# Optimization experiments

Hardware: AMD Instinct MI355X
Metric: run time of the kernel (lower is better)

The kernel has to match this reference:

```python
import jax, jax.numpy as jnp
import numpy as np

B, N, M, D_IN, D_OUT, H = 4, 2048, 2048, 512, 512, 8
HD = D_OUT // H
LN_EPS = 1e-5


def setup_inputs() -> dict:
    key = jax.random.key(0)
    ks = jax.random.split(key, 10)
    query = jax.random.normal(ks[0], (B, N, D_IN), dtype=jnp.float32)
    kee = jax.random.normal(ks[1], (B, M, D_IN), dtype=jnp.float32)
    val = jax.random.normal(ks[2], (B, M, D_IN), dtype=jnp.float32)
    mask = jax.random.randint(ks[3], (B, N, M), 0, 2, dtype=jnp.int32)
    # xavier_uniform with gain 1/sqrt(2): limit = gain * sqrt(6/(fan_in+fan_out))
    lim = (1.0 / np.sqrt(2.0)) * np.sqrt(6.0 / (D_IN + D_OUT))
    WQ = jax.random.uniform(ks[4], (D_OUT, D_IN), jnp.float32, -lim, lim)
    WK = jax.random.uniform(ks[5], (D_OUT, D_IN), jnp.float32, -lim, lim)
    WV = jax.random.uniform(ks[6], (D_OUT, D_IN), jnp.float32, -lim, lim)
    limO = (1.0 / np.sqrt(2.0)) * np.sqrt(6.0 / (D_OUT + D_OUT))
    WO = jax.random.uniform(ks[7], (D_OUT, D_OUT), jnp.float32, -limO, limO)
    bO = jnp.zeros((D_OUT,), jnp.float32)
    gamma = jnp.ones((D_OUT,), jnp.float32)
    beta = jnp.zeros((D_OUT,), jnp.float32)
    return {"query": query, "key": kee, "value": val, "mask": mask,
            "WQ": WQ, "WK": WK, "WV": WV, "WO": WO, "bO": bO,
            "gamma": gamma, "beta": beta}


def reference(query, key, value, mask, WQ, WK, WV, WO, bO, gamma, beta):
    scale = jnp.float32(1.0 / np.sqrt(HD))
    # project and split heads: [B, H, S, HD]
    Q = (query @ WQ.T).reshape(B, N, H, HD).transpose(0, 2, 1, 3)
    K = (key @ WK.T).reshape(B, M, H, HD).transpose(0, 2, 1, 3)
    V = (value @ WV.T).reshape(B, M, H, HD).transpose(0, 2, 1, 3)
    attn = jnp.einsum('bhnd,bhmd->bhnm', Q, K) * scale
    attn = jnp.where(mask[:, None, :, :] == 0, -jnp.inf, attn)
    attn = jax.nn.softmax(attn, axis=-1)  # dropout is identity in eval
    out = jnp.einsum('bhnm,bhmd->bhnd', attn, V)
    out = out.transpose(0, 2, 1, 3).reshape(B, N, D_OUT)
    out = out @ WO.T + bO
    x = out + query  # residual_proj is Identity (input_dim == output_dim)
    mu = jnp.mean(x, axis=-1, keepdims=True)
    var = jnp.var(x, axis=-1, keepdims=True)
    return (x - mu) * jax.lax.rsqrt(var + LN_EPS) * gamma + beta
```

## Files before the change

### kernel.cpp

```cpp
#include <hip/hip_runtime.h>
#include <stdint.h>

#define B_   4
#define N_   2048
#define M_   2048
#define DIN  512
#define DOUT 512
#define H_   8
#define HD_  64
#define ROWS (B_ * N_)

typedef __attribute__((ext_vector_type(8))) short bf16x8;
typedef __attribute__((ext_vector_type(4))) float f32x4;
typedef __attribute__((ext_vector_type(2))) unsigned int u32x2;
typedef __attribute__((ext_vector_type(4))) unsigned short u16x4;
typedef unsigned short u16;
typedef unsigned int   u32;

#if __has_builtin(__builtin_amdgcn_exp2f)
#define EXP2(x) __builtin_amdgcn_exp2f(x)
#else
#define EXP2(x) exp2f(x)
#endif

__device__ __forceinline__ u16 f2bf(float x) {
  union { float f; u32 u; } v; v.f = x;
  u32 r = (v.u + 0x7FFFu + ((v.u >> 16) & 1u)) >> 16;
  return (u16)r;
}

__device__ __forceinline__ float bf2f(u16 x) {
  union { u32 u; float f; } v; v.u = ((u32)x) << 16;
  return v.f;
}

__device__ __forceinline__ u32 pkbf(float a, float b) {
  u32 r;
  asm("v_cvt_pk_bf16_f32 %0, %1, %2" : "=v"(r) : "v"(a), "v"(b));
  return r;
}

__device__ __forceinline__ void gld16(u16* lds, const u16* g) {
  __builtin_amdgcn_global_load_lds((const __attribute__((address_space(1))) u32*)g,
                                   (__attribute__((address_space(3))) u32*)lds, 16, 0, 0);
}

__global__ __launch_bounds__(256) void k_prep(
    const float* __restrict__ q, const float* __restrict__ k, const float* __restrict__ v,
    const float* __restrict__ wq_, const float* __restrict__ wk_,
    const float* __restrict__ wv_, const float* __restrict__ wo_,
    const int* __restrict__ mask,
    u16* __restrict__ qb, u16* __restrict__ kb, u16* __restrict__ vb,
    u16* __restrict__ wqb, u16* __restrict__ wkb, u16* __restrict__ wvb, u16* __restrict__ wob,
    u32* __restrict__ mbits)
{
  const int id = blockIdx.x;
  if (id >= 6656) {
    const int id2 = id - 6656;
    const int lane = threadIdx.x & 63;
    const int gw = id2 * 4 + (threadIdx.x >> 6);
    #pragma unroll
    for (int it2 = 0; it2 < 4; ++it2) {
      long pos = ((long)gw * 4 + it2) * 64 + lane;
      int mv = mask[pos];
      unsigned long long bal = __ballot(mv != 0);
      if ((lane & 31) == 0) mbits[pos >> 5] = (u32)(bal >> lane);
    }
    return;
  }
  const float* s; u16* d; size_t i;
  if (id < 6144) {
    const int seg = id >> 11;
    s = seg == 0 ? q : seg == 1 ? k : v;
    d = seg == 0 ? qb : seg == 1 ? kb : vb;
    i = (size_t)(id & 2047) * 2048 + threadIdx.x * 8;
  } else {
    const int wid = id - 6144;
    const int seg = wid >> 7;
    s = seg == 0 ? wq_ : seg == 1 ? wk_ : seg == 2 ? wv_ : wo_;
    d = seg == 0 ? wqb : seg == 1 ? wkb : seg == 2 ? wvb : wob;
    i = (size_t)(wid & 127) * 2048 + threadIdx.x * 8;
  }
  f32x4 x = *(const f32x4*)(s + i);
  f32x4 y = *(const f32x4*)(s + i + 4);
  bf16x8 r;
  r[0] = (short)f2bf(x[0]); r[1] = (short)f2bf(x[1]);
  r[2] = (short)f2bf(x[2]); r[3] = (short)f2bf(x[3]);
  r[4] = (short)f2bf(y[0]); r[5] = (short)f2bf(y[1]);
  r[6] = (short)f2bf(y[2]); r[7] = (short)f2bf(y[3]);
  *(bf16x8*)(d + i) = r;
}

__global__ __launch_bounds__(256) void k_gemm_qkv(
    const u16* __restrict__ Aq, const u16* __restrict__ Ak, const u16* __restrict__ Av,
    const u16* __restrict__ Wq, const u16* __restrict__ Wk, const u16* __restrict__ Wv,
    u16* __restrict__ Qo, u16* __restrict__ Ko, u16* __restrict__ Vt)
{
  __shared__ __align__(16) u16 At[2][128 * 64];
  __shared__ __align__(16) u16 Bt[2][128 * 64];
  const int z = blockIdx.z;
  const u16* A = z == 0 ? Aq : z == 1 ? Ak : Av;
  const u16* W = z == 0 ? Wq : z == 1 ? Wk : Wv;
  const int bm = blockIdx.y, bn = blockIdx.x;
  const int t = threadIdx.x, l = t & 63;
  const int w = t >> 6, wr = w >> 1, wc = w & 1;
  const int l15 = l & 15, lg = l >> 4;
  f32x4 acc[4][4] = {};
  const u16* ga = A + (size_t)(bm * 128 + (t >> 3)) * DIN + (t & 7) * 8;
  const u16* gb = W + (size_t)(bn * 128 + (t >> 3)) * DIN + (t & 7) * 8;

  #define STG(buf_, k0_) do {                                           \
    u16* la_ = &At[buf_][t * 8];                                        \
    u16* lb_ = &Bt[buf_][t * 8];                                        \
    _Pragma("unroll")                                                   \
    for (int s2 = 0; s2 < 4; ++s2) {                                    \
      gld16(la_ + s2 * 2048, ga + (size_t)s2 * 32 * DIN + (k0_));       \
      gld16(lb_ + s2 * 2048, gb + (size_t)s2 * 32 * DIN + (k0_));       \
    }                                                                   \
  } while (0)

  STG(0, 0);
  __syncthreads();
  for (int kt = 0; kt < 8; ++kt) {
    const int buf = kt & 1;
    if (kt + 1 < 8) STG(buf ^ 1, (kt + 1) * 64);
    const u16* rowT = (z < 2) ? &Bt[buf][wc * 64 * 64] : &At[buf][wr * 64 * 64];
    const u16* colT = (z < 2) ? &At[buf][wr * 64 * 64] : &Bt[buf][wc * 64 * 64];
    bf16x8 rf[4][2], cf[4][2];
    #pragma unroll
    for (int i = 0; i < 4; ++i)
      #pragma unroll
      for (int c = 0; c < 2; ++c)
        rf[i][c] = *(const bf16x8*)&rowT[(i * 16 + l15) * 64 + c * 32 + lg * 8];
    #pragma unroll
    for (int j = 0; j < 4; ++j)
      #pragma unroll
      for (int c = 0; c < 2; ++c)
        cf[j][c] = *(const bf16x8*)&colT[(j * 16 + l15) * 64 + c * 32 + lg * 8];
    #pragma unroll
    for (int i = 0; i < 4; ++i)
      #pragma unroll
      for (int j = 0; j < 4; ++j) {
        acc[i][j] = __builtin_amdgcn_mfma_f32_16x16x32_bf16(rf[i][0], cf[j][0], acc[i][j], 0, 0, 0);
        acc[i][j] = __builtin_amdgcn_mfma_f32_16x16x32_bf16(rf[i][1], cf[j][1], acc[i][j], 0, 0, 0);
      }
    __syncthreads();
  }
  #undef STG
  if (z < 2) {
    u16* C = z == 0 ? Qo : Ko;
    const float scl = z == 0 ? 0.18033688f : 1.0f;
    #pragma unroll
    for (int i = 0; i < 4; ++i) {
      const int o0 = bn * 128 + wc * 64 + i * 16 + lg * 4;
      #pragma unroll
      for (int j = 0; j < 4; ++j) {
        const int m = bm * 128 + wr * 64 + j * 16 + l15;
        u32x2 pr;
        pr[0] = pkbf(acc[i][j][0] * scl, acc[i][j][1] * scl);
        pr[1] = pkbf(acc[i][j][2] * scl, acc[i][j][3] * scl);
        *(u32x2*)&C[(size_t)m * DOUT + o0] = pr;
      }
    }
  } else {
    #pragma unroll
    for (int i = 0; i < 4; ++i) {
      const int mm = bm * 128 + wr * 64 + i * 16 + lg * 4;
      const int bb = mm >> 11, s = mm & 2047;
      #pragma unroll
      for (int j = 0; j < 4; ++j) {
        const int o = bn * 128 + wc * 64 + j * 16 + l15;
        u32x2 pr;
        pr[0] = pkbf(acc[i][j][0], acc[i][j][1]);
        pr[1] = pkbf(acc[i][j][2], acc[i][j][3]);
        *(u32x2*)&Vt[(size_t)(bb * 512 + o) * M_ + s] = pr;
      }
    }
  }
}

__global__ __launch_bounds__(256) void k_attn(
    const u16* __restrict__ Qp, const u16* __restrict__ Kp, const u16* __restrict__ Vt,
    const u32* __restrict__ mbits, u16* __restrict__ AO)
{
  __shared__ __align__(16) u16 KT[3][64 * 64];
  __shared__ __align__(16) u16 VT[3][64 * 64];
  const int qt = blockIdx.x, bh = blockIdx.y;
  const int b = bh >> 3, h = bh & 7;
  const int t = threadIdx.x, l = t & 63, w = t >> 6;
  const int l15 = l & 15, lg = l >> 4;

  const int srow = t >> 3;
  const int scol8 = t & 7;
  const int scol = (scol8 ^ (srow & 7)) * 8;
  const int kpr = (srow >> 5) * 32 + (((srow >> 4) & 1) * 4) + (((srow & 15) >> 2) * 8) + (srow & 3);
  const u16* gK = Kp + (size_t)(b * N_ + kpr) * DOUT + h * HD_ + scol;
  const u16* gV = Vt + (size_t)(b * 512 + h * HD_ + srow) * M_ + scol;

  const int qrow = qt * 64 + w * 16 + l15;
  const bf16x8 qf0 = *(const bf16x8*)&Qp[((size_t)(b * N_) + qrow) * DOUT + h * HD_ + lg * 8];
  const bf16x8 qf1 = *(const bf16x8*)&Qp[((size_t)(b * N_) + qrow) * DOUT + h * HD_ + 32 + lg * 8];
  const u32* mrow = mbits + ((size_t)(b * N_) + qrow) * (M_ / 32);

  f32x4 o[4] = {};
  f32x4 lacc = {};
  union U8 { u32 u[4]; bf16x8 v; };
  U8 ones;
  ones.u[0] = ones.u[1] = ones.u[2] = ones.u[3] = 0x3F803F80u;

  #define STAGE(buf_, m0_) do {                                   \
    const u16* gk_ = gK + (size_t)(m0_) * DOUT;                   \
    const u16* gv_ = gV + (m0_);                                  \
    u16* lk_ = &KT[buf_][t * 8];                                  \
    u16* lv_ = &VT[buf_][t * 8];                                  \
    gld16(lk_, gk_);                                              \
    gld16(lk_ + 2048, gk_ + (size_t)32 * DOUT);                   \
    gld16(lv_, gv_);                                              \
    gld16(lv_ + 2048, gv_ + (size_t)32 * M_);                     \
  } while (0)

  u32x2 mc = *(const u32x2*)&mrow[0];
  STAGE(0, 0);
  STAGE(1, 64);
  __builtin_amdgcn_sched_barrier(0);
  asm volatile("s_waitcnt vmcnt(4)" ::: "memory");
  __builtin_amdgcn_sched_barrier(0);
  __builtin_amdgcn_s_barrier();
  __builtin_amdgcn_sched_barrier(0);

  for (int it = 0; it < 32; ++it) {
    const int cur = it % 3;
    const u16* Kb = KT[cur];
    const u16* Vb = VT[cur];

    u32x2 mn = {0u, 0u};
    if (it + 1 < 32) mn = *(const u32x2*)&mrow[2 * (it + 1)];
    if (it + 2 < 32) STAGE((it + 2) % 3, (it + 2) * 64);
    __builtin_amdgcn_sched_barrier(0);

    const int xs = l15 & 7;
    U8 pa[2];
    #pragma unroll
    for (int kbk = 0; kbk < 2; ++kbk) {
      f32x4 sS[2];
      #pragma unroll
      for (int u = 0; u < 2; ++u) {
        const int row = kbk * 32 + u * 16 + l15;
        const bf16x8 a0 = *(const bf16x8*)&Kb[row * 64 + ((lg ^ xs) * 8)];
        const bf16x8 a1 = *(const bf16x8*)&Kb[row * 64 + (((4 + lg) ^ xs) * 8)];
        f32x4 zz = {};
        zz = __builtin_amdgcn_mfma_f32_16x16x32_bf16(a0, qf0, zz, 0, 0, 0);
        zz = __builtin_amdgcn_mfma_f32_16x16x32_bf16(a1, qf1, zz, 0, 0, 0);
        sS[u] = zz;
      }
      const u32 mw = kbk ? mc[1] : mc[0];
      float e[8];
      #pragma unroll
      for (int u = 0; u < 2; ++u)
        #pragma unroll
        for (int r = 0; r < 4; ++r) {
          const int bit = lg * 8 + u * 4 + r;
          float p = EXP2(sS[u][r]);
          e[u * 4 + r] = ((mw >> bit) & 1u) ? p : 0.f;
        }
      pa[kbk].u[0] = pkbf(e[0], e[1]);
      pa[kbk].u[1] = pkbf(e[2], e[3]);
      pa[kbk].u[2] = pkbf(e[4], e[5]);
      pa[kbk].u[3] = pkbf(e[6], e[7]);
    }
    lacc = __builtin_amdgcn_mfma_f32_16x16x32_bf16(ones.v, pa[0].v, lacc, 0, 0, 0);
    lacc = __builtin_amdgcn_mfma_f32_16x16x32_bf16(ones.v, pa[1].v, lacc, 0, 0, 0);
    #pragma unroll
    for (int nd = 0; nd < 4; ++nd) {
      const int vrow = nd * 16 + l15;
      const bf16x8 vb0 = *(const bf16x8*)&Vb[vrow * 64 + ((lg ^ xs) * 8)];
      const bf16x8 vb1 = *(const bf16x8*)&Vb[vrow * 64 + (((4 + lg) ^ xs) * 8)];
      o[nd] = __builtin_amdgcn_mfma_f32_16x16x32_bf16(vb0, pa[0].v, o[nd], 0, 0, 0);
      o[nd] = __builtin_amdgcn_mfma_f32_16x16x32_bf16(vb1, pa[1].v, o[nd], 0, 0, 0);
    }
    mc = mn;

    __builtin_amdgcn_sched_barrier(0);
    if (it < 30) {
      asm volatile("s_waitcnt vmcnt(5)" ::: "memory");
      __builtin_amdgcn_sched_barrier(0);
      __builtin_amdgcn_s_barrier();
      __builtin_amdgcn_sched_barrier(0);
    } else if (it == 30) {
      asm volatile("s_waitcnt vmcnt(1)" ::: "memory");
      __builtin_amdgcn_sched_barrier(0);
      __builtin_amdgcn_s_barrier();
      __builtin_amdgcn_sched_barrier(0);
    }
  }

  const float ls = lacc[0];
  const float rq = ls > 0.f ? 1.f / ls : 0.f;
  const size_t obase = ((size_t)(b * N_) + qrow) * DOUT + h * HD_;
  #pragma unroll
  for (int nd = 0; nd < 4; ++nd) {
    u32x2 pr;
    pr[0] = pkbf(o[nd][0] * rq, o[nd][1] * rq);
    pr[1] = pkbf(o[nd][2] * rq, o[nd][3] * rq);
    *(u32x2*)&AO[obase + nd * 16 + lg * 4] = pr;
  }
  #undef STAGE
}

__global__ __launch_bounds__(256) void k_gemm_out(
    const u16* __restrict__ A, const u16* __restrict__ W,
    const float* __restrict__ bO, const u16* __restrict__ qb,
    u16* __restrict__ X)
{
  __shared__ __align__(16) u16 At[2][128 * 64];
  __shared__ __align__(16) u16 Bt[2][128 * 64];
  const int bm = blockIdx.y, bn = blockIdx.x;
  const int t = threadIdx.x, l = t & 63;
  const int w = t >> 6, wr = w >> 1, wc = w & 1;
  const int l15 = l & 15, lg = l >> 4;
  f32x4 acc[4][4] = {};
  const u16* ga = A + (size_t)(bm * 128 + (t >> 3)) * DOUT + (t & 7) * 8;
  const u16* gb = W + (size_t)(bn * 128 + (t >> 3)) * DOUT + (t & 7) * 8;

  #define STG(buf_, k0_) do {                                           \
    u16* la_ = &At[buf_][t * 8];                                        \
    u16* lb_ = &Bt[buf_][t * 8];                                        \
    _Pragma("unroll")                                                   \
    for (int s2 = 0; s2 < 4; ++s2) {                                    \
      gld16(la_ + s2 * 2048, ga + (size_t)s2 * 32 * DOUT + (k0_));      \
      gld16(lb_ + s2 * 2048, gb + (size_t)s2 * 32 * DOUT + (k0_));      \
    }                                                                   \
  } while (0)

  STG(0, 0);
  __syncthreads();
  for (int kt = 0; kt < 8; ++kt) {
    const int buf = kt & 1;
    if (kt + 1 < 8) STG(buf ^ 1, (kt + 1) * 64);
    const u16* rowT = &Bt[buf][wc * 64 * 64];
    const u16* colT = &At[buf][wr * 64 * 64];
    bf16x8 rf[4][2], cf[4][2];
    #pragma unroll
    for (int i = 0; i < 4; ++i)
      #pragma unroll
      for (int c = 0; c < 2; ++c)
        rf[i][c] = *(const bf16x8*)&rowT[(i * 16 + l15) * 64 + c * 32 + lg * 8];
    #pragma unroll
    for (int j = 0; j < 4; ++j)
      #pragma unroll
      for (int c = 0; c < 2; ++c)
        cf[j][c] = *(const bf16x8*)&colT[(j * 16 + l15) * 64 + c * 32 + lg * 8];
    #pragma unroll
    for (int i = 0; i < 4; ++i)
      #pragma unroll
      for (int j = 0; j < 4; ++j) {
        acc[i][j] = __builtin_amdgcn_mfma_f32_16x16x32_bf16(rf[i][0], cf[j][0], acc[i][j], 0, 0, 0);
        acc[i][j] = __builtin_amdgcn_mfma_f32_16x16x32_bf16(rf[i][1], cf[j][1], acc[i][j], 0, 0, 0);
      }
    __syncthreads();
  }
  #undef STG
  #pragma unroll
  for (int i = 0; i < 4; ++i) {
    const int o0 = bn * 128 + wc * 64 + i * 16 + lg * 4;
    const f32x4 bo4 = *(const f32x4*)&bO[o0];
    #pragma unroll
    for (int j = 0; j < 4; ++j) {
      const int m = bm * 128 + wr * 64 + j * 16 + l15;
      const size_t idx = (size_t)m * DOUT + o0;
      const u16x4 qv = *(const u16x4*)&qb[idx];
      u32x2 pr;
      pr[0] = pkbf(acc[i][j][0] + bo4[0] + bf2f(qv[0]), acc[i][j][1] + bo4[1] + bf2f(qv[1]));
      pr[1] = pkbf(acc[i][j][2] + bo4[2] + bf2f(qv[2]), acc[i][j][3] + bo4[3] + bf2f(qv[3]));
      *(u32x2*)&X[idx] = pr;
    }
  }
}

__global__ __launch_bounds__(256) void k_ln(
    const u16* __restrict__ X, const float* __restrict__ gamma,
    const float* __restrict__ beta, float* __restrict__ out)
{
  const int w = threadIdx.x >> 6, l = threadIdx.x & 63;
  const int row = blockIdx.x * 4 + w;
  const bf16x8 xv = *(const bf16x8*)(X + (size_t)row * DOUT + l * 8);
  float xf[8];
  #pragma unroll
  for (int i = 0; i < 8; ++i) xf[i] = bf2f((u16)xv[i]);
  float s = 0.f, q = 0.f;
  #pragma unroll
  for (int i = 0; i < 8; ++i) { s += xf[i]; q += xf[i] * xf[i]; }
  #pragma unroll
  for (int m = 1; m < 64; m <<= 1) { s += __shfl_xor(s, m); q += __shfl_xor(q, m); }
  const float mean = s * (1.f / 512.f);
  const float var = q * (1.f / 512.f) - mean * mean;
  const float rstd = rsqrtf(var + 1e-5f);
  f32x4 g1 = *(const f32x4*)(gamma + l * 8);
  f32x4 g2 = *(const f32x4*)(gamma + l * 8 + 4);
  f32x4 e1 = *(const f32x4*)(beta + l * 8);
  f32x4 e2 = *(const f32x4*)(beta + l * 8 + 4);
  f32x4 r1, r2;
  #pragma unroll
  for (int i = 0; i < 4; ++i) {
    r1[i] = (xf[i] - mean) * rstd * g1[i] + e1[i];
    r2[i] = (xf[i + 4] - mean) * rstd * g2[i] + e2[i];
  }
  float* op = out + (size_t)row * DOUT + l * 8;
  *(f32x4*)(op) = r1;
  *(f32x4*)(op + 4) = r2;
}

extern "C" void kernel_launch(void* const* d_in, const int* in_sizes, int n_in,
                              void* d_out, int out_size, void* d_ws, size_t ws_size,
                              hipStream_t stream)
{
  const float* query = (const float*)d_in[0];
  const float* key   = (const float*)d_in[1];
  const float* value = (const float*)d_in[2];
  const int*   mask  = (const int*)d_in[3];
  const float* WQ    = (const float*)d_in[4];
  const float* WK    = (const float*)d_in[5];
  const float* WV    = (const float*)d_in[6];
  const float* WO    = (const float*)d_in[7];
  const float* bO    = (const float*)d_in[8];
  const float* gamma = (const float*)d_in[9];
  const float* beta  = (const float*)d_in[10];
  float* out = (float*)d_out;

  char* ws = (char*)d_ws;
  size_t off = 0;
  auto alloc = [&](size_t bytes) -> char* {
    char* p = ws + off;
    off += (bytes + 255) & ~(size_t)255;
    return p;
  };
  u16* qb  = (u16*)alloc((size_t)ROWS * DIN * 2);
  u16* kb  = (u16*)alloc((size_t)ROWS * DIN * 2);
  u16* vb  = (u16*)alloc((size_t)ROWS * DIN * 2);
  u16* wq  = (u16*)alloc((size_t)DOUT * DIN * 2);
  u16* wk  = (u16*)alloc((size_t)DOUT * DIN * 2);
  u16* wv  = (u16*)alloc((size_t)DOUT * DIN * 2);
  u16* wo  = (u16*)alloc((size_t)DOUT * DIN * 2);
  u16* Qp  = (u16*)alloc((size_t)ROWS * DOUT * 2);
  u16* Kp  = (u16*)alloc((size_t)ROWS * DOUT * 2);
  u16* Vt  = (u16*)alloc((size_t)ROWS * DOUT * 2);
  u32* mb  = (u32*)alloc((size_t)B_ * N_ * (M_ / 32) * 4);
  u16* AO  = vb;
  u16* X   = kb;

  k_prep     <<<23040, 256, 0, stream>>>(query, key, value, WQ, WK, WV, WO, mask,
                                         qb, kb, vb, wq, wk, wv, wo, mb);
  k_gemm_qkv <<<dim3(4, 64, 3), 256, 0, stream>>>(qb, kb, vb, wq, wk, wv, Qp, Kp, Vt);
  k_attn     <<<dim3(32, 32), 256, 0, stream>>>(Qp, Kp, Vt, mb, AO);
  k_gemm_out <<<dim3(4, 64), 256, 0, stream>>>(AO, wo, bO, qb, X);
  k_ln       <<<2048, 256, 0, stream>>>(X, gamma, beta, out);
}
```

Baseline: 287.1 us.

## Enlarge attention blocks, simplify double-buffered pipeline, swizzle grids across XCDs

Attention blocks grow to 512 threads covering 128 query rows, so each staged K/V tile is shared by twice as many waves. The 3-stage pipeline with manual waitcnt is replaced by a simple double buffer with __syncthreads. s_setprio is raised around MFMA sections, and mask words are now loaded in the same iteration instead of one ahead. All three kernels switch to 1-D grids with an XCD-aware block index swizzle meant to improve L2 locality, at the cost of less load/compute overlap in the attention loop.

```diff
diff --git a/kernel.cpp b/kernel.cpp
--- a/kernel.cpp
+++ b/kernel.cpp
@@ -98,10 +98,11 @@
 {
   __shared__ __align__(16) u16 At[2][128 * 64];
   __shared__ __align__(16) u16 Bt[2][128 * 64];
-  const int z = blockIdx.z;
+  const int swz = (blockIdx.x & 7) * 96 + (blockIdx.x >> 3);
+  const int z = swz >> 8;
+  const int bm = (swz & 255) >> 2, bn = swz & 3;
   const u16* A = z == 0 ? Aq : z == 1 ? Ak : Av;
   const u16* W = z == 0 ? Wq : z == 1 ? Wk : Wv;
-  const int bm = blockIdx.y, bn = blockIdx.x;
   const int t = threadIdx.x, l = t & 63;
   const int w = t >> 6, wr = w >> 1, wc = w & 1;
   const int l15 = l & 15, lg = l >> 4;
@@ -179,13 +180,14 @@
   }
 }
 
-__global__ __launch_bounds__(256) void k_attn(
+__global__ __launch_bounds__(512, 4) void k_attn(
     const u16* __restrict__ Qp, const u16* __restrict__ Kp, const u16* __restrict__ Vt,
     const u32* __restrict__ mbits, u16* __restrict__ AO)
 {
-  __shared__ __align__(16) u16 KT[3][64 * 64];
-  __shared__ __align__(16) u16 VT[3][64 * 64];
-  const int qt = blockIdx.x, bh = blockIdx.y;
+  __shared__ __align__(16) u16 KT[2][64 * 64];
+  __shared__ __align__(16) u16 VT[2][64 * 64];
+  const int swz = (blockIdx.x & 7) * 64 + (blockIdx.x >> 3);
+  const int qt = swz & 15, bh = swz >> 4;
   const int b = bh >> 3, h = bh & 7;
   const int t = threadIdx.x, l = t & 63, w = t >> 6;
   const int l15 = l & 15, lg = l >> 4;
@@ -197,7 +199,7 @@
   const u16* gK = Kp + (size_t)(b * N_ + kpr) * DOUT + h * HD_ + scol;
   const u16* gV = Vt + (size_t)(b * 512 + h * HD_ + srow) * M_ + scol;
 
-  const int qrow = qt * 64 + w * 16 + l15;
+  const int qrow = qt * 128 + w * 16 + l15;
   const bf16x8 qf0 = *(const bf16x8*)&Qp[((size_t)(b * N_) + qrow) * DOUT + h * HD_ + lg * 8];
   const bf16x8 qf1 = *(const bf16x8*)&Qp[((size_t)(b * N_) + qrow) * DOUT + h * HD_ + 32 + lg * 8];
   const u32* mrow = mbits + ((size_t)(b * N_) + qrow) * (M_ / 32);
@@ -209,40 +211,28 @@
   ones.u[0] = ones.u[1] = ones.u[2] = ones.u[3] = 0x3F803F80u;
 
   #define STAGE(buf_, m0_) do {                                   \
-    const u16* gk_ = gK + (size_t)(m0_) * DOUT;                   \
-    const u16* gv_ = gV + (m0_);                                  \
-    u16* lk_ = &KT[buf_][t * 8];                                  \
-    u16* lv_ = &VT[buf_][t * 8];                                  \
-    gld16(lk_, gk_);                                              \
-    gld16(lk_ + 2048, gk_ + (size_t)32 * DOUT);                   \
-    gld16(lv_, gv_);                                              \
-    gld16(lv_ + 2048, gv_ + (size_t)32 * M_);                     \
+    gld16(&KT[buf_][t * 8], gK + (size_t)(m0_) * DOUT);           \
+    gld16(&VT[buf_][t * 8], gV + (m0_));                          \
   } while (0)
 
-  u32x2 mc = *(const u32x2*)&mrow[0];
   STAGE(0, 0);
-  STAGE(1, 64);
-  __builtin_amdgcn_sched_barrier(0);
-  asm volatile("s_waitcnt vmcnt(4)" ::: "memory");
-  __builtin_amdgcn_sched_barrier(0);
-  __builtin_amdgcn_s_barrier();
-  __builtin_amdgcn_sched_barrier(0);
+  __syncthreads();
 
   for (int it = 0; it < 32; ++it) {
-    const int cur = it % 3;
-    const u16* Kb = KT[cur];
-    const u16* Vb = VT[cur];
-
-    u32x2 mn = {0u, 0u};
-    if (it + 1 < 32) mn = *(const u32x2*)&mrow[2 * (it + 1)];
-    if (it + 2 < 32) STAGE((it + 2) % 3, (it + 2) * 64);
-    __builtin_amdgcn_sched_barrier(0);
-
+    const int buf = it & 1;
+    const int m0 = it * 64;
+    if (it + 1 < 32) STAGE(buf ^ 1, m0 + 64);
+
+    const u32x2 mc = *(const u32x2*)&mrow[2 * it];
+    const u16* Kb = KT[buf];
+    const u16* Vb = VT[buf];
     const int xs = l15 & 7;
+
     U8 pa[2];
     #pragma unroll
     for (int kbk = 0; kbk < 2; ++kbk) {
       f32x4 sS[2];
+      __builtin_amdgcn_s_setprio(1);
       #pragma unroll
       for (int u = 0; u < 2; ++u) {
         const int row = kbk * 32 + u * 16 + l15;
@@ -253,6 +243,7 @@
         zz = __builtin_amdgcn_mfma_f32_16x16x32_bf16(a1, qf1, zz, 0, 0, 0);
         sS[u] = zz;
       }
+      __builtin_amdgcn_s_setprio(0);
       const u32 mw = kbk ? mc[1] : mc[0];
       float e[8];
       #pragma unroll
@@ -268,6 +259,7 @@
       pa[kbk].u[2] = pkbf(e[4], e[5]);
       pa[kbk].u[3] = pkbf(e[6], e[7]);
     }
+    __builtin_amdgcn_s_setprio(1);
     lacc = __builtin_amdgcn_mfma_f32_16x16x32_bf16(ones.v, pa[0].v, lacc, 0, 0, 0);
     lacc = __builtin_amdgcn_mfma_f32_16x16x32_bf16(ones.v, pa[1].v, lacc, 0, 0, 0);
     #pragma unroll
@@ -278,20 +270,8 @@
       o[nd] = __builtin_amdgcn_mfma_f32_16x16x32_bf16(vb0, pa[0].v, o[nd], 0, 0, 0);
       o[nd] = __builtin_amdgcn_mfma_f32_16x16x32_bf16(vb1, pa[1].v, o[nd], 0, 0, 0);
     }
-    mc = mn;
-
-    __builtin_amdgcn_sched_barrier(0);
-    if (it < 30) {
-      asm volatile("s_waitcnt vmcnt(5)" ::: "memory");
-      __builtin_amdgcn_sched_barrier(0);
-      __builtin_amdgcn_s_barrier();
-      __builtin_amdgcn_sched_barrier(0);
-    } else if (it == 30) {
-      asm volatile("s_waitcnt vmcnt(1)" ::: "memory");
-      __builtin_amdgcn_sched_barrier(0);
-      __builtin_amdgcn_s_barrier();
-      __builtin_amdgcn_sched_barrier(0);
-    }
+    __builtin_amdgcn_s_setprio(0);
+    __syncthreads();
   }
 
   const float ls = lacc[0];
@@ -314,7 +294,8 @@
 {
   __shared__ __align__(16) u16 At[2][128 * 64];
   __shared__ __align__(16) u16 Bt[2][128 * 64];
-  const int bm = blockIdx.y, bn = blockIdx.x;
+  const int swz = (blockIdx.x & 7) * 32 + (blockIdx.x >> 3);
+  const int bm = swz >> 2, bn = swz & 3;
   const int t = threadIdx.x, l = t & 63;
   const int w = t >> 6, wr = w >> 1, wc = w & 1;
   const int l15 = l & 15, lg = l >> 4;
@@ -450,8 +431,8 @@
 
   k_prep     <<<23040, 256, 0, stream>>>(query, key, value, WQ, WK, WV, WO, mask,
                                          qb, kb, vb, wq, wk, wv, wo, mb);
-  k_gemm_qkv <<<dim3(4, 64, 3), 256, 0, stream>>>(qb, kb, vb, wq, wk, wv, Qp, Kp, Vt);
-  k_attn     <<<dim3(32, 32), 256, 0, stream>>>(Qp, Kp, Vt, mb, AO);
-  k_gemm_out <<<dim3(4, 64), 256, 0, stream>>>(AO, wo, bO, qb, X);
+  k_gemm_qkv <<<768, 256, 0, stream>>>(qb, kb, vb, wq, wk, wv, Qp, Kp, Vt);
+  k_attn     <<<512, 512, 0, stream>>>(Qp, Kp, Vt, mb, AO);
+  k_gemm_out <<<256, 256, 0, stream>>>(AO, wo, bO, qb, X);
   k_ln       <<<2048, 256, 0, stream>>>(X, gamma, beta, out);
 }
```

Result: faster. 263.3 us (-8.3%).
